# Performance work log

Measured on AMD Instinct MI355X. Metric: run time of the kernel, lower is better.

The kernel has to match this reference:

```python
import jax, jax.numpy as jnp
import numpy as np

N, B, CIN = 2048, 16, 1
M = 4096
COUT = 64
R = 128


def setup_inputs() -> dict:
    key = jax.random.key(0)
    k1, k2, k3, k4, k5 = jax.random.split(key, 5)
    return {
        "context_in": jax.random.normal(k1, (N, B, CIN), dtype=jnp.float32),
        "context_out": jax.random.normal(k2, (N, B, COUT), dtype=jnp.float32),
        "target_in": jax.random.normal(k3, (M, B, CIN), dtype=jnp.float32),
        "lengthscale": jnp.ones((1,), dtype=jnp.float32),
        "W": jax.random.normal(k4, (R, COUT + 1), dtype=jnp.float32),
        "b": jax.random.normal(k5, (R,), dtype=jnp.float32),
    }


def reference(context_in, context_out, target_in, lengthscale, W, b):
    # context_in: (N,B,Cin), context_out: (N,B,Cout), target_in: (M,B,Cin)
    n, batch, _ = context_in.shape
    # density channel prepended -> (N,B,Cout+1)
    dens = jnp.ones((n, batch, 1), dtype=context_in.dtype)
    co = jnp.concatenate([dens, context_out], axis=-1)
    ci = jnp.transpose(context_in, (1, 0, 2))   # (B,N,Cin)
    ti = jnp.transpose(target_in, (1, 0, 2))    # (B,M,Cin)
    # squared pairwise distances (B,N,M)
    d2 = (jnp.sum(ci * ci, -1)[:, :, None]
          + jnp.sum(ti * ti, -1)[:, None, :]
          - 2.0 * jnp.einsum('bnd,bmd->bnm', ci, ti))
    d2 = jnp.maximum(d2, 0.0)
    # RBF kernel: exp(-0.5 * d2 / lengthscale^2)
    K = jnp.exp(-0.5 * d2 / (lengthscale[0] ** 2))  # (B,N,M)
    # weighted sum over context points: (B,M,Cout+1)
    out = jnp.einsum('nbc,bnm->bmc', co, K)
    # density normalization of non-density channels
    out = jnp.concatenate([out[..., :1], out[..., 1:] / (out[..., :1] + 1e-8)], axis=-1)
    # linear projection (Cout+1 -> R)
    out = out @ W.T + b
    return jnp.transpose(out, (1, 0, 2))  # (M,B,R)
```

## Files before the change

kernel.cpp:

```cpp
#include <hip/hip_runtime.h>
#include <hip/hip_bf16.h>


#define N_CTX 2048
#define BATCH 16
#define M_TGT 4096
#define COUT  64
#define RDIM  128

#define WS_CO_BYTES (N_CTX * BATCH * COUT * 2)
#define WS_SXA_OFF  WS_CO_BYTES
#define WS_SXB_OFF  (WS_SXA_OFF + N_CTX * BATCH * 4)
#define WS_WT_OFF   (WS_SXB_OFF + N_CTX * BATCH * 4)

#define SSCALE 0.8493222f

typedef __attribute__((ext_vector_type(8)))  short        bf16x8;
typedef __attribute__((ext_vector_type(4)))  float        floatx4;
typedef __attribute__((ext_vector_type(4)))  unsigned int uint4v;

#if __has_builtin(__builtin_amdgcn_exp2f)
#define EXP2F __builtin_amdgcn_exp2f
#else
#define EXP2F exp2f
#endif

static __device__ __forceinline__ unsigned int pack_bf16(float lo, float hi) {
    __hip_bfloat162 h = __float22bfloat162_rn(make_float2(lo, hi));
    return *reinterpret_cast<unsigned int*>(&h);
}
static __device__ __forceinline__ unsigned short f2bf(float f) {
    __hip_bfloat16 h = __float2bfloat16(f);
    return *reinterpret_cast<unsigned short*>(&h);
}

__global__ __launch_bounds__(256)
void convdeepset_prep(const float* __restrict__ ci, const float* __restrict__ co,
                      const float* __restrict__ ls, const float* __restrict__ W,
                      unsigned char* __restrict__ ws)
{
    unsigned short* cow = (unsigned short*)ws;
    float*          sxa = (float*)(ws + WS_SXA_OFF);
    float*          sxb = (float*)(ws + WS_SXB_OFF);
    unsigned short* wt  = (unsigned short*)(ws + WS_WT_OFF);
    const int blk = blockIdx.x, tid = threadIdx.x;

    if (blk < 1024) {
        const int g    = blk * 4 + (tid >> 6);
        const int bb   = g & 15;
        const int nblk = g >> 4;
        const int c    = tid & 63;
        const float* rp = co + ((size_t)nblk * 8 * BATCH + bb) * COUT + c;
        unsigned int u[4];
#pragma unroll
        for (int j = 0; j < 4; ++j) {
            const float f0 = rp[(size_t)(2 * j)     * BATCH * COUT];
            const float f1 = rp[(size_t)(2 * j + 1) * BATCH * COUT];
            u[j] = pack_bf16(f0, f1);
        }
        *(uint4v*)&cow[(size_t)bb * 131072 + nblk * 512 + c * 8] = *(uint4v*)u;
    } else if (blk < 1152) {
        const int f = (blk - 1024) * 256 + tid;
        const int n = f & 2047, bb = f >> 11;
        const float s = SSCALE / ls[0];
        const float v = s * ci[(size_t)n * BATCH + bb];
        sxa[bb * 2048 + n] = v + v;
        sxb[bb * 2048 + n] = -v * v;
    } else {
        for (int f = tid; f < 8192; f += 256) {
            const int cp = f & 7, r = (f >> 3) & 127, ch = f >> 10;
            wt[ch * 1024 + r * 8 + cp] = f2bf(W[r * 65 + 1 + ch * 8 + cp]);
        }
    }
}

struct Slot {
    bf16x8  c0, c1, c2, c3;
    floatx4 xa0, xa1, xb0, xb1;
};

__global__ __launch_bounds__(256)
void convdeepset_main(const float* __restrict__ ti, const float* __restrict__ ls,
                      const float* __restrict__ W,  const float* __restrict__ bias,
                      const unsigned char* __restrict__ ws, float* __restrict__ out)
{
    __shared__ unsigned short vstage[4][2][1024];

    const int tid  = threadIdx.x;
    const int lane = tid & 63;
    const int wv   = tid >> 6;
    const int g2   = lane >> 4;
    const int l15  = lane & 15;

    const int xcd = blockIdx.x & 7;
    const int i   = blockIdx.x >> 3;
    const int b   = xcd * 2 + (i & 1);
    const int mt  = i >> 1;
    const int m0  = mt * 128 + wv * 32;

    const float s   = SSCALE / ls[0];
    const float sy0 = s * ti[(size_t)(m0 + l15) * BATCH + b];
    const float sy1 = s * ti[(size_t)(m0 + 16 + l15) * BATCH + b];

    const unsigned short* cowb = (const unsigned short*)ws + (size_t)b * 131072;
    const float* sxa = (const float*)(ws + WS_SXA_OFF) + b * N_CTX;
    const float* sxb = (const float*)(ws + WS_SXB_OFF) + b * N_CTX;

    const short onebf = (short)0x3F80;
    bf16x8 ones;
#pragma unroll
    for (int j = 0; j < 8; ++j) ones[j] = onebf;

    floatx4 acc0[4], acc1[4], accd0, accd1;
#pragma unroll
    for (int q = 0; q < 4; ++q)
#pragma unroll
        for (int e = 0; e < 4; ++e) { acc0[q][e] = 0.0f; acc1[q][e] = 0.0f; }
#pragma unroll
    for (int e = 0; e < 4; ++e) { accd0[e] = 0.0f; accd1[e] = 0.0f; }

    auto loadk = [&](Slot& S, int k) {
        const unsigned short* bp = cowb + ((k * 4 + g2) << 9) + l15 * 8;
        S.c0 = *(const bf16x8*)(bp);
        S.c1 = *(const bf16x8*)(bp + 128);
        S.c2 = *(const bf16x8*)(bp + 256);
        S.c3 = *(const bf16x8*)(bp + 384);
        const float* ap  = sxa + k * 32 + g2 * 8;
        const float* bpx = sxb + k * 32 + g2 * 8;
        S.xa0 = *(const floatx4*)(ap);
        S.xa1 = *(const floatx4*)(ap + 4);
        S.xb0 = *(const floatx4*)(bpx);
        S.xb1 = *(const floatx4*)(bpx + 4);
    };

    auto compute = [&](const Slot& S) {
        const floatx4 a00 = S.xa0 * sy0 + S.xb0;
        const floatx4 a01 = S.xa1 * sy0 + S.xb1;
        const floatx4 a10 = S.xa0 * sy1 + S.xb0;
        const floatx4 a11 = S.xa1 * sy1 + S.xb1;
        float kv0[8], kv1[8];
        kv0[0] = EXP2F(a00.x); kv0[1] = EXP2F(a00.y);
        kv0[2] = EXP2F(a00.z); kv0[3] = EXP2F(a00.w);
        kv0[4] = EXP2F(a01.x); kv0[5] = EXP2F(a01.y);
        kv0[6] = EXP2F(a01.z); kv0[7] = EXP2F(a01.w);
        kv1[0] = EXP2F(a10.x); kv1[1] = EXP2F(a10.y);
        kv1[2] = EXP2F(a10.z); kv1[3] = EXP2F(a10.w);
        kv1[4] = EXP2F(a11.x); kv1[5] = EXP2F(a11.y);
        kv1[6] = EXP2F(a11.z); kv1[7] = EXP2F(a11.w);
        uint4v aw0, aw1;
#pragma unroll
        for (int q = 0; q < 4; ++q) {
            aw0[q] = pack_bf16(kv0[2 * q], kv0[2 * q + 1]);
            aw1[q] = pack_bf16(kv1[2 * q], kv1[2 * q + 1]);
        }
        const bf16x8 av0 = __builtin_bit_cast(bf16x8, aw0);
        const bf16x8 av1 = __builtin_bit_cast(bf16x8, aw1);
        acc0[0] = __builtin_amdgcn_mfma_f32_16x16x32_bf16(av0, S.c0, acc0[0], 0, 0, 0);
        acc0[1] = __builtin_amdgcn_mfma_f32_16x16x32_bf16(av0, S.c1, acc0[1], 0, 0, 0);
        acc0[2] = __builtin_amdgcn_mfma_f32_16x16x32_bf16(av0, S.c2, acc0[2], 0, 0, 0);
        acc0[3] = __builtin_amdgcn_mfma_f32_16x16x32_bf16(av0, S.c3, acc0[3], 0, 0, 0);
        accd0   = __builtin_amdgcn_mfma_f32_16x16x32_bf16(av0, ones, accd0, 0, 0, 0);
        acc1[0] = __builtin_amdgcn_mfma_f32_16x16x32_bf16(av1, S.c0, acc1[0], 0, 0, 0);
        acc1[1] = __builtin_amdgcn_mfma_f32_16x16x32_bf16(av1, S.c1, acc1[1], 0, 0, 0);
        acc1[2] = __builtin_amdgcn_mfma_f32_16x16x32_bf16(av1, S.c2, acc1[2], 0, 0, 0);
        acc1[3] = __builtin_amdgcn_mfma_f32_16x16x32_bf16(av1, S.c3, acc1[3], 0, 0, 0);
        accd1   = __builtin_amdgcn_mfma_f32_16x16x32_bf16(av1, ones, accd1, 0, 0, 0);
    };

    Slot A, B;
    loadk(A, 0);
    for (int p = 0; p < 64; p += 2) {
        loadk(B, p + 1);
        compute(A);
        if (p + 2 < 64) loadk(A, p + 2);
        compute(B);
    }

    const unsigned short* wtg = (const unsigned short*)(ws + WS_WT_OFF);
    const float sy0sq = sy0 * sy0;
    const float sy1sq = sy1 * sy1;
#pragma unroll
    for (int tile = 0; tile < 2; ++tile) {
        const floatx4* acc  = tile ? acc1 : acc0;
        const floatx4  accd = tile ? accd1 : accd0;
        const float    sysq = tile ? sy1sq : sy0sq;
        float dt[4], ff[4];
#pragma unroll
        for (int reg = 0; reg < 4; ++reg) {
            const int m   = (lane >> 4) * 4 + reg;
            const float ysq = __shfl(sysq, m, 64);
            const float e   = EXP2F(-ysq);
            dt[reg] = accd[reg] * e;
            ff[reg] = e / (dt[reg] + 1e-8f);
        }
        unsigned short* vs = vstage[wv][tile];
#pragma unroll
        for (int reg = 0; reg < 4; ++reg) {
            const int m = (lane >> 4) * 4 + reg;
#pragma unroll
            for (int q = 0; q < 4; ++q) {
                const int c = q * 16 + l15;
                vs[(c >> 3) * 128 + m * 8 + (c & 7)] = f2bf(acc[q][reg]);
            }
        }
        floatx4 pacc[8];
#pragma unroll
        for (int rt = 0; rt < 8; ++rt)
#pragma unroll
            for (int e = 0; e < 4; ++e) pacc[rt][e] = 0.0f;
#pragma unroll
        for (int s2 = 0; s2 < 2; ++s2) {
            const int ch = s2 * 4 + g2;
            const bf16x8 avp = *(const bf16x8*)&vs[ch * 128 + l15 * 8];
#pragma unroll
            for (int rt = 0; rt < 8; ++rt) {
                const bf16x8 bvp = *(const bf16x8*)&wtg[ch * 1024 + (rt * 16 + l15) * 8];
                pacc[rt] = __builtin_amdgcn_mfma_f32_16x16x32_bf16(avp, bvp, pacc[rt], 0, 0, 0);
            }
        }
#pragma unroll
        for (int rt = 0; rt < 8; ++rt) {
            const int r = rt * 16 + l15;
            const float w0v = W[r * 65];
            const float bv  = bias[r];
#pragma unroll
            for (int reg = 0; reg < 4; ++reg) {
                const int m = (lane >> 4) * 4 + reg;
                out[((size_t)(m0 + tile * 16 + m) * BATCH + b) * RDIM + r]
                    = pacc[rt][reg] * ff[reg] + dt[reg] * w0v + bv;
            }
        }
    }
}

extern "C" void kernel_launch(void* const* d_in, const int* in_sizes, int n_in,
                              void* d_out, int out_size, void* d_ws, size_t ws_size,
                              hipStream_t stream) {
    const float* ci   = (const float*)d_in[0];
    const float* co   = (const float*)d_in[1];
    const float* ti   = (const float*)d_in[2];
    const float* ls   = (const float*)d_in[3];
    const float* W    = (const float*)d_in[4];
    const float* bias = (const float*)d_in[5];
    float* o = (float*)d_out;
    (void)in_sizes; (void)n_in; (void)out_size; (void)ws_size;

    convdeepset_prep<<<1153, 256, 0, stream>>>(ci, co, ls, W, (unsigned char*)d_ws);
    convdeepset_main<<<512, 256, 0, stream>>>(
        ti, ls, W, bias, (const unsigned char*)d_ws, o);
}
```

Before: 129.7 us.

## Split context reduction across wave pairs and double grid size

Each block now covers 64 targets instead of 128. Each pair of waves splits the 2048 context points in half, and the partial accumulators are combined through shared memory before the projection. This doubles the grid to 1024 blocks, which raises parallelism and occupancy (launch bounds also request 4 blocks per CU) and halves each wave's serial K-loop. In exchange it adds an LDS reduction, a block-wide barrier, and more shared memory per block.

```diff
diff --git a/kernel.cpp b/kernel.cpp
--- a/kernel.cpp
+++ b/kernel.cpp
@@ -79,32 +79,36 @@
     floatx4 xa0, xa1, xb0, xb1;
 };
 
-__global__ __launch_bounds__(256)
+__global__ __launch_bounds__(256, 4)
 void convdeepset_main(const float* __restrict__ ti, const float* __restrict__ ls,
                       const float* __restrict__ W,  const float* __restrict__ bias,
                       const unsigned char* __restrict__ ws, float* __restrict__ out)
 {
-    __shared__ unsigned short vstage[4][2][1024];
+    __shared__ float xred[4][64][20];
+    __shared__ unsigned short vstage[4][1024];
 
     const int tid  = threadIdx.x;
     const int lane = tid & 63;
     const int wv   = tid >> 6;
     const int g2   = lane >> 4;
     const int l15  = lane & 15;
+    const int wpr  = wv >> 1;
+    const int half = wv & 1;
 
     const int xcd = blockIdx.x & 7;
     const int i   = blockIdx.x >> 3;
     const int b   = xcd * 2 + (i & 1);
     const int mt  = i >> 1;
-    const int m0  = mt * 128 + wv * 32;
+    const int m0  = mt * 64 + wpr * 32;
 
     const float s   = SSCALE / ls[0];
     const float sy0 = s * ti[(size_t)(m0 + l15) * BATCH + b];
     const float sy1 = s * ti[(size_t)(m0 + 16 + l15) * BATCH + b];
 
-    const unsigned short* cowb = (const unsigned short*)ws + (size_t)b * 131072;
-    const float* sxa = (const float*)(ws + WS_SXA_OFF) + b * N_CTX;
-    const float* sxb = (const float*)(ws + WS_SXB_OFF) + b * N_CTX;
+    const unsigned short* cowb = (const unsigned short*)ws
+                               + (size_t)b * 131072 + (size_t)half * 65536;
+    const float* sxa = (const float*)(ws + WS_SXA_OFF) + b * N_CTX + half * 1024;
+    const float* sxb = (const float*)(ws + WS_SXB_OFF) + b * N_CTX + half * 1024;
 
     const short onebf = (short)0x3F80;
     bf16x8 ones;
@@ -169,66 +173,81 @@
 
     Slot A, B;
     loadk(A, 0);
-    for (int p = 0; p < 64; p += 2) {
+    for (int p = 0; p < 32; p += 2) {
         loadk(B, p + 1);
         compute(A);
-        if (p + 2 < 64) loadk(A, p + 2);
+        if (p + 2 < 32) loadk(A, p + 2);
         compute(B);
     }
 
+    {
+        float* xw = &xred[wv][lane][0];
+        const floatx4* wacc = half ? acc0 : acc1;
+        const floatx4  wd   = half ? accd0 : accd1;
+#pragma unroll
+        for (int q = 0; q < 4; ++q) *(floatx4*)&xw[q * 4] = wacc[q];
+        *(floatx4*)&xw[16] = wd;
+    }
+    __syncthreads();
+    floatx4  facc[4];
+    floatx4  faccd;
+    {
+        const float* xr = &xred[wv ^ 1][lane][0];
+        const floatx4* kacc = half ? acc1 : acc0;
+        const floatx4  kd   = half ? accd1 : accd0;
+#pragma unroll
+        for (int q = 0; q < 4; ++q) facc[q] = kacc[q] + *(const floatx4*)&xr[q * 4];
+        faccd = kd + *(const floatx4*)&xr[16];
+    }
+
     const unsigned short* wtg = (const unsigned short*)(ws + WS_WT_OFF);
-    const float sy0sq = sy0 * sy0;
-    const float sy1sq = sy1 * sy1;
-#pragma unroll
-    for (int tile = 0; tile < 2; ++tile) {
-        const floatx4* acc  = tile ? acc1 : acc0;
-        const floatx4  accd = tile ? accd1 : accd0;
-        const float    sysq = tile ? sy1sq : sy0sq;
-        float dt[4], ff[4];
-#pragma unroll
-        for (int reg = 0; reg < 4; ++reg) {
-            const int m   = (lane >> 4) * 4 + reg;
-            const float ysq = __shfl(sysq, m, 64);
-            const float e   = EXP2F(-ysq);
-            dt[reg] = accd[reg] * e;
-            ff[reg] = e / (dt[reg] + 1e-8f);
-        }
-        unsigned short* vs = vstage[wv][tile];
+    const float sysq = half ? sy1 * sy1 : sy0 * sy0;
+    const int   mrow = m0 + half * 16;
+
+    float dt[4], ff[4];
+#pragma unroll
+    for (int reg = 0; reg < 4; ++reg) {
+        const int m   = (lane >> 4) * 4 + reg;
+        const float ysq = __shfl(sysq, m, 64);
+        const float e   = EXP2F(-ysq);
+        dt[reg] = faccd[reg] * e;
+        ff[reg] = e / (dt[reg] + 1e-8f);
+    }
+    unsigned short* vs = vstage[wv];
+#pragma unroll
+    for (int reg = 0; reg < 4; ++reg) {
+        const int m = (lane >> 4) * 4 + reg;
+#pragma unroll
+        for (int q = 0; q < 4; ++q) {
+            const int c = q * 16 + l15;
+            vs[(c >> 3) * 128 + m * 8 + (c & 7)] = f2bf(facc[q][reg]);
+        }
+    }
+    floatx4 pacc[8];
+#pragma unroll
+    for (int rt = 0; rt < 8; ++rt)
+#pragma unroll
+        for (int e = 0; e < 4; ++e) pacc[rt][e] = 0.0f;
+#pragma unroll
+    for (int s2 = 0; s2 < 2; ++s2) {
+        const int ch = s2 * 4 + g2;
+        const bf16x8 avp = *(const bf16x8*)&vs[ch * 128 + l15 * 8];
+#pragma unroll
+        for (int rt = 0; rt < 8; ++rt) {
+            const bf16x8 bvp = *(const bf16x8*)&wtg[ch * 1024 + (rt * 16 + l15) * 8];
+            pacc[rt] = __builtin_amdgcn_mfma_f32_16x16x32_bf16(avp, bvp, pacc[rt], 0, 0, 0);
+        }
+    }
+#pragma unroll
+    for (int rt = 0; rt < 8; ++rt) {
+        const int r = rt * 16 + l15;
+        const float w0v = W[r * 65];
+        const float bv  = bias[r];
 #pragma unroll
         for (int reg = 0; reg < 4; ++reg) {
             const int m = (lane >> 4) * 4 + reg;
-#pragma unroll
-            for (int q = 0; q < 4; ++q) {
-                const int c = q * 16 + l15;
-                vs[(c >> 3) * 128 + m * 8 + (c & 7)] = f2bf(acc[q][reg]);
-            }
-        }
-        floatx4 pacc[8];
-#pragma unroll
-        for (int rt = 0; rt < 8; ++rt)
-#pragma unroll
-            for (int e = 0; e < 4; ++e) pacc[rt][e] = 0.0f;
-#pragma unroll
-        for (int s2 = 0; s2 < 2; ++s2) {
-            const int ch = s2 * 4 + g2;
-            const bf16x8 avp = *(const bf16x8*)&vs[ch * 128 + l15 * 8];
-#pragma unroll
-            for (int rt = 0; rt < 8; ++rt) {
-                const bf16x8 bvp = *(const bf16x8*)&wtg[ch * 1024 + (rt * 16 + l15) * 8];
-                pacc[rt] = __builtin_amdgcn_mfma_f32_16x16x32_bf16(avp, bvp, pacc[rt], 0, 0, 0);
-            }
-        }
-#pragma unroll
-        for (int rt = 0; rt < 8; ++rt) {
-            const int r = rt * 16 + l15;
-            const float w0v = W[r * 65];
-            const float bv  = bias[r];
-#pragma unroll
-            for (int reg = 0; reg < 4; ++reg) {
-                const int m = (lane >> 4) * 4 + reg;
-                out[((size_t)(m0 + tile * 16 + m) * BATCH + b) * RDIM + r]
-                    = pacc[rt][reg] * ff[reg] + dt[reg] * w0v + bv;
-            }
+            out[((size_t)(mrow + m) * BATCH + b) * RDIM + r]
+                = pacc[rt][reg] * ff[reg] + dt[reg] * w0v + bv;
         }
     }
 }
@@ -246,6 +265,6 @@
     (void)in_sizes; (void)n_in; (void)out_size; (void)ws_size;
 
     convdeepset_prep<<<1153, 256, 0, stream>>>(ci, co, ls, W, (unsigned char*)d_ws);
-    convdeepset_main<<<512, 256, 0, stream>>>(
+    convdeepset_main<<<1024, 256, 0, stream>>>(
         ti, ls, W, bias, (const unsigned char*)d_ws, o);
 }
```

New measurement: 128.5 us. No clear change (-0.9%).
